# Optimization experiments

Hardware: AMD Instinct MI355X
Metric: run time of the kernel (lower is better)

Reference implementation:

```python
import jax, jax.numpy as jnp
import numpy as np
import math

HEADS = 16
HEAD_DIM = 64
MODEL_DIM = HEADS * HEAD_DIM
SEQ = 2048
BATCH = 2


def setup_inputs() -> dict:
    key = jax.random.key(0)
    ks = jax.random.split(key, 11)
    s = 0.02
    return {
        "query": jax.random.normal(ks[0], (SEQ, BATCH, MODEL_DIM), jnp.float32),
        "key": jax.random.normal(ks[1], (SEQ, BATCH, MODEL_DIM), jnp.float32),
        "value": jax.random.normal(ks[2], (SEQ, BATCH, MODEL_DIM), jnp.float32),
        "mask": jnp.ones((1, SEQ, 1), jnp.int32),
        "Wq": jax.random.normal(ks[3], (MODEL_DIM, MODEL_DIM), jnp.float32) * s,
        "bq": jax.random.normal(ks[4], (MODEL_DIM,), jnp.float32) * s,
        "Wk": jax.random.normal(ks[5], (MODEL_DIM, MODEL_DIM), jnp.float32) * s,
        "bk": jax.random.normal(ks[6], (MODEL_DIM,), jnp.float32) * s,
        "Wv": jax.random.normal(ks[7], (MODEL_DIM, MODEL_DIM), jnp.float32) * s,
        "bv": jax.random.normal(ks[8], (MODEL_DIM,), jnp.float32) * s,
        "Wo": jax.random.normal(ks[9], (MODEL_DIM, MODEL_DIM), jnp.float32) * s,
        "bo": jax.random.normal(ks[10], (MODEL_DIM,), jnp.float32) * s,
    }


def _proj(x, W, b):
    # torch nn.Linear: y = x @ W.T + b ; then view to [.., H, D]
    y = jnp.einsum("sbm,nm->sbn", x, W) + b
    return y.reshape(x.shape[0], x.shape[1], HEADS, HEAD_DIM)


def reference(query, key, value, mask, Wq, bq, Wk, bk, Wv, bv, Wo, bo):
    # NOTE: original module applies mask to `score` AFTER softmax has been
    # taken, and the masked score is discarded -> mask has no effect.
    del mask
    seq_len, batch_size, _ = query.shape
    scale = 1.0 / math.sqrt(HEAD_DIM)
    q = _proj(query, Wq, bq)   # [S,B,H,D]
    k = _proj(key, Wk, bk)
    v = _proj(value, Wv, bv)
    score = jnp.einsum("ibhd,jbhd->ijbh", q, k) * scale  # [S,S,B,H]
    attn = jax.nn.softmax(score, axis=1)  # softmax over key axis j
    # dropout: eval-mode identity (deterministic baseline)
    x = jnp.einsum("ijbh,jbhd->ibhd", attn, v)
    x = x.reshape(seq_len, batch_size, MODEL_DIM)
    return jnp.einsum("sbm,nm->sbn", x, Wo) + bo
```

## Files before the change

kernel.cpp:

```cpp
#include <hip/hip_runtime.h>

#define SEQ    2048
#define NBATCH 2
#define NHEAD  16
#define HD     64
#define MD     1024
#define TOK    (SEQ * NBATCH)
#define XN8    (TOK * MD / 8)
#define WN8    (MD * MD / 8)

typedef __attribute__((ext_vector_type(4)))  float f32x4;
typedef __attribute__((ext_vector_type(16))) float f32x16;
typedef __attribute__((ext_vector_type(8)))  short bf16x8;
typedef __attribute__((ext_vector_type(8)))  unsigned short u16x8;

__device__ __forceinline__ unsigned short f2bf(float f) {
  union { float f; unsigned int u; } x; x.f = f;
  unsigned int u = x.u + 0x7fffu + ((x.u >> 16) & 1u);
  return (unsigned short)(u >> 16);
}

__device__ __forceinline__ unsigned cvtpk(float lo, float hi) {
  unsigned r;
  asm("v_cvt_pk_bf16_f32 %0, %1, %2" : "=v"(r) : "v"(lo), "v"(hi));
  return r;
}
__device__ __forceinline__ void plswap(unsigned &a, unsigned &b) {
  asm volatile("v_permlane32_swap_b32 %0, %1" : "+v"(a), "+v"(b));
}

__device__ __forceinline__ void gload_lds16(const void* g, void* l) {
  typedef const __attribute__((address_space(1))) unsigned int* gp_t;
  typedef __attribute__((address_space(3))) unsigned int* lp_t;
  __builtin_amdgcn_global_load_lds((gp_t)g, (lp_t)l, 16, 0, 0);
}

__global__ __launch_bounds__(256) void cvt_all(
    const float* __restrict__ q, const float* __restrict__ k, const float* __restrict__ v,
    const float* __restrict__ wq, const float* __restrict__ wk,
    const float* __restrict__ wv, const float* __restrict__ wo,
    unsigned short* __restrict__ oq, unsigned short* __restrict__ ok,
    unsigned short* __restrict__ ov, unsigned short* __restrict__ owq,
    unsigned short* __restrict__ owk, unsigned short* __restrict__ owv,
    unsigned short* __restrict__ owo) {
  const int i = blockIdx.x * 256 + threadIdx.x;
  const float* src; unsigned short* dst; int r;
  if (i < 3 * XN8) {
    const int s = i >> 19; r = i & (XN8 - 1);
    src = s == 0 ? q : (s == 1 ? k : v);
    dst = s == 0 ? oq : (s == 1 ? ok : ov);
  } else {
    const int j = i - 3 * XN8; const int s = j >> 17; r = j & (WN8 - 1);
    src = s == 0 ? wq : (s == 1 ? wk : (s == 2 ? wv : wo));
    dst = s == 0 ? owq : (s == 1 ? owk : (s == 2 ? owv : owo));
  }
  const float4* p = (const float4*)src + (size_t)r * 2;
  float4 a = p[0];
  float4 b = p[1];
  u16x8 o;
  o[0] = f2bf(a.x); o[1] = f2bf(a.y); o[2] = f2bf(a.z); o[3] = f2bf(a.w);
  o[4] = f2bf(b.x); o[5] = f2bf(b.y); o[6] = f2bf(b.z); o[7] = f2bf(b.w);
  *((u16x8*)dst + r) = o;
}

__global__ __launch_bounds__(512) void gemm_qkv(
    const unsigned short* __restrict__ Xq, const unsigned short* __restrict__ Xk,
    const unsigned short* __restrict__ Xv, const unsigned short* __restrict__ Wq,
    const unsigned short* __restrict__ Wk, const unsigned short* __restrict__ Wv,
    const float* __restrict__ bq, const float* __restrict__ bk, const float* __restrict__ bv,
    unsigned short* __restrict__ Qo, unsigned short* __restrict__ Ko,
    unsigned short* __restrict__ Vo, float qscale) {
  __shared__ unsigned short sA[3][128 * 32];
  __shared__ unsigned short sB[3][128 * 32];
  const int tid  = threadIdx.x;
  const int lane = tid & 63;
  const int wave = tid >> 6;
  const int wm   = (wave >> 2) << 6;
  const int wn   = (wave & 3) << 5;
  const int l15  = lane & 15;
  const int g    = lane >> 4;
  const int z    = blockIdx.z;

  const unsigned short* A; const unsigned short* B; const float* bias;
  int bM, bN;
  if (z == 0)      { A = Xq; B = Wq; bias = bq; }
  else if (z == 1) { A = Xk; B = Wk; bias = bk; }
  else             { A = Wv; B = Xv; bias = bv; }
  if (z < 2) { bM = blockIdx.y << 7; bN = blockIdx.x << 7; }
  else       { bM = blockIdx.x << 7; bN = blockIdx.y << 7; }

  f32x4 acc[4][2];
#pragma unroll
  for (int a_ = 0; a_ < 4; ++a_)
#pragma unroll
    for (int b_ = 0; b_ < 2; ++b_)
      acc[a_][b_] = f32x4{0.f, 0.f, 0.f, 0.f};

  const int r = tid >> 2, cc = tid & 3;

  auto stage = [&](int c, int kt) {
    const int k0 = kt << 5;
    gload_lds16(A + (size_t)(bM + r) * MD + k0 + cc * 8, (char*)sA[c] + tid * 16);
    gload_lds16(B + (size_t)(bN + r) * MD + k0 + cc * 8, (char*)sB[c] + tid * 16);
  };

  const int nk = MD >> 5;
  stage(0, 0);
  stage(1, 1);
  asm volatile("s_waitcnt vmcnt(2)" ::: "memory");
  __builtin_amdgcn_s_barrier();

  int cur = 0;
  for (int kt = 0; kt < nk; ++kt) {
    if (kt + 2 < nk) stage(cur == 0 ? 2 : cur - 1, kt + 2);
    bf16x8 af[4], bfr[2];
#pragma unroll
    for (int f = 0; f < 4; ++f)
      af[f] = *(const bf16x8*)&sA[cur][(wm + f * 16 + l15) * 32 + g * 8];
#pragma unroll
    for (int f = 0; f < 2; ++f)
      bfr[f] = *(const bf16x8*)&sB[cur][(wn + f * 16 + l15) * 32 + g * 8];
#pragma unroll
    for (int mf = 0; mf < 4; ++mf)
#pragma unroll
      for (int nf = 0; nf < 2; ++nf)
        acc[mf][nf] = __builtin_amdgcn_mfma_f32_16x16x32_bf16(af[mf], bfr[nf], acc[mf][nf], 0, 0, 0);
    if (kt + 2 < nk)
      asm volatile("s_waitcnt vmcnt(2)" ::: "memory");
    else if (kt + 1 < nk)
      asm volatile("s_waitcnt vmcnt(0)" ::: "memory");
    if (kt + 1 < nk) __builtin_amdgcn_s_barrier();
    cur = (cur == 2) ? 0 : cur + 1;
  }

  if (z < 2) {
    unsigned short* O = (z == 0) ? Qo : Ko;
    const float scale = (z == 0) ? qscale : 1.0f;
#pragma unroll
    for (int nf = 0; nf < 2; ++nf) {
      const int cch = bN + wn + nf * 16 + l15;
      const float bb = bias[cch];
      const int h = cch >> 6, d = cch & 63;
#pragma unroll
      for (int mf = 0; mf < 4; ++mf)
#pragma unroll
        for (int i = 0; i < 4; ++i) {
          const int t = bM + wm + mf * 16 + (g << 2) + i;
          const int b = t & 1, s = t >> 1;
          O[((((b << 4) + h) * SEQ + s) << 6) + d] = f2bf((acc[mf][nf][i] + bb) * scale);
        }
    }
  } else {
#pragma unroll
    for (int mf = 0; mf < 4; ++mf)
#pragma unroll
      for (int i = 0; i < 4; ++i) {
        const int rch = bM + wm + mf * 16 + (g << 2) + i;
        const float bb = bias[rch];
        const int h = rch >> 6, d = rch & 63;
#pragma unroll
        for (int nf = 0; nf < 2; ++nf) {
          const int t = bN + wn + nf * 16 + l15;
          const int b = t & 1, s = t >> 1;
          Vo[((((b << 4) + h) << 6) + d) * SEQ + s] = f2bf(acc[mf][nf][i] + bb);
        }
      }
  }
}

__global__ __launch_bounds__(512) void gemm_oproj(const unsigned short* __restrict__ A,
                                                  const unsigned short* __restrict__ B,
                                                  const float* __restrict__ bias,
                                                  float* __restrict__ O) {
  __shared__ unsigned short sA[3][128 * 32];
  __shared__ unsigned short sB[3][128 * 32];
  const int tid  = threadIdx.x;
  const int lane = tid & 63;
  const int wave = tid >> 6;
  const int wm   = (wave >> 2) << 6;
  const int wn   = (wave & 3) << 5;
  const int l15  = lane & 15;
  const int g    = lane >> 4;
  const int bM   = blockIdx.y << 7;
  const int bN   = blockIdx.x << 7;

  f32x4 acc[4][2];
#pragma unroll
  for (int a_ = 0; a_ < 4; ++a_)
#pragma unroll
    for (int b_ = 0; b_ < 2; ++b_)
      acc[a_][b_] = f32x4{0.f, 0.f, 0.f, 0.f};

  const int r = tid >> 2, cc = tid & 3;
  auto stage = [&](int c, int kt) {
    const int k0 = kt << 5;
    gload_lds16(A + (size_t)(bM + r) * MD + k0 + cc * 8, (char*)sA[c] + tid * 16);
    gload_lds16(B + (size_t)(bN + r) * MD + k0 + cc * 8, (char*)sB[c] + tid * 16);
  };

  const int nk = MD >> 5;
  stage(0, 0);
  stage(1, 1);
  asm volatile("s_waitcnt vmcnt(2)" ::: "memory");
  __builtin_amdgcn_s_barrier();

  int cur = 0;
  for (int kt = 0; kt < nk; ++kt) {
    if (kt + 2 < nk) stage(cur == 0 ? 2 : cur - 1, kt + 2);
    bf16x8 af[4], bfr[2];
#pragma unroll
    for (int f = 0; f < 4; ++f)
      af[f] = *(const bf16x8*)&sA[cur][(wm + f * 16 + l15) * 32 + g * 8];
#pragma unroll
    for (int f = 0; f < 2; ++f)
      bfr[f] = *(const bf16x8*)&sB[cur][(wn + f * 16 + l15) * 32 + g * 8];
#pragma unroll
    for (int mf = 0; mf < 4; ++mf)
#pragma unroll
      for (int nf = 0; nf < 2; ++nf)
        acc[mf][nf] = __builtin_amdgcn_mfma_f32_16x16x32_bf16(af[mf], bfr[nf], acc[mf][nf], 0, 0, 0);
    if (kt + 2 < nk)
      asm volatile("s_waitcnt vmcnt(2)" ::: "memory");
    else if (kt + 1 < nk)
      asm volatile("s_waitcnt vmcnt(0)" ::: "memory");
    if (kt + 1 < nk) __builtin_amdgcn_s_barrier();
    cur = (cur == 2) ? 0 : cur + 1;
  }

#pragma unroll
  for (int nf = 0; nf < 2; ++nf) {
    const int cch = bN + wn + nf * 16 + l15;
    const float bb = bias[cch];
#pragma unroll
    for (int mf = 0; mf < 4; ++mf)
#pragma unroll
      for (int i = 0; i < 4; ++i) {
        const int t = bM + wm + mf * 16 + (g << 2) + i;
        O[(size_t)t * MD + cch] = acc[mf][nf][i] + bb;
      }
  }
}

__global__ __launch_bounds__(512) void attn_fwd(const unsigned short* __restrict__ Qg,
                                                const unsigned short* __restrict__ Kg,
                                                const unsigned short* __restrict__ Vg,
                                                unsigned short* __restrict__ Xout) {
  __shared__ unsigned short sK[2][2][64 * 64];
  __shared__ unsigned short sV[2][2][64 * 64];

  const int tid  = threadIdx.x;
  const int lane = tid & 63;
  const int wave = tid >> 6;
  const int ws   = wave & 3;
  const int grp  = wave >> 2;
  const int l31  = lane & 31;
  const int half = lane >> 5;
  const int bh   = blockIdx.y;
  const int q0w  = (blockIdx.x << 7) + (ws << 5);

  const unsigned short* Qb = Qg + (size_t)bh * (SEQ * HD);
  const char* Kb = (const char*)(Kg + (size_t)bh * (SEQ * HD));
  const char* Vb = (const char*)(Vg + (size_t)bh * (HD * SEQ));

  bf16x8 qf[4];
#pragma unroll
  for (int c = 0; c < 4; ++c)
    qf[c] = *(const bf16x8*)&Qb[(size_t)(q0w + l31) * HD + c * 16 + half * 8];

  f32x16 acc_o[2];
#pragma unroll
  for (int dt = 0; dt < 2; ++dt)
#pragma unroll
    for (int e = 0; e < 16; ++e) acc_o[dt][e] = 0.f;
  float lrow = 0.f;

  auto stage = [&](int c, int kt) {
#pragma unroll
    for (int h = 0; h < 2; ++h) {
      const int p = tid << 4;
      const int row = p >> 7;
      const int lcol = (p ^ ((row & 7) << 4)) & 127;
      const int kbase = (h << 10) + (kt << 6);
      gload_lds16(Kb + (size_t)(kbase + row) * (HD * 2) + lcol,
                  (char*)sK + ((h * 2 + c) << 13) + p);
      gload_lds16(Vb + (size_t)row * (SEQ * 2) + (kbase << 1) + lcol,
                  (char*)sV + ((h * 2 + c) << 13) + p);
    }
  };

  const char* myK = (char*)sK + (grp << 14);
  const char* myV = (char*)sV + (grp << 14);

  stage(0, 0);
  __syncthreads();
  int cur = 0;

  const int NT = SEQ / 2 / 64;
  for (int kt = 0; kt < NT; ++kt) {
    if (kt + 1 < NT) stage(cur ^ 1, kt + 1);

    f32x16 accs[2];
    __builtin_amdgcn_s_setprio(1);
#pragma unroll
    for (int ks = 0; ks < 2; ++ks) {
#pragma unroll
      for (int e = 0; e < 16; ++e) accs[ks][e] = 0.f;
      const int krow = ks * 32 + l31;
      const int swz  = (krow & 7) << 4;
#pragma unroll
      for (int c = 0; c < 4; ++c) {
        const int off = (krow << 7) + ((c * 32 + half * 16) ^ swz);
        bf16x8 kf = *(const bf16x8*)(myK + (cur << 13) + off);
        accs[ks] = __builtin_amdgcn_mfma_f32_32x32x16_bf16(kf, qf[c], accs[ks], 0, 0, 0);
      }
    }
    __builtin_amdgcn_s_setprio(0);

    float rsum = 0.f;
#pragma unroll
    for (int ks = 0; ks < 2; ++ks)
#pragma unroll
      for (int e = 0; e < 16; ++e) {
        const float pv = __builtin_amdgcn_exp2f(accs[ks][e]);
        accs[ks][e] = pv;
        rsum += pv;
      }
    lrow += rsum;

    bf16x8 pa[4];
#pragma unroll
    for (int ks = 0; ks < 2; ++ks)
#pragma unroll
      for (int hc = 0; hc < 2; ++hc) {
        const int b = hc * 8;
        unsigned X  = cvtpk(accs[ks][b + 0], accs[ks][b + 1]);
        unsigned X2 = cvtpk(accs[ks][b + 2], accs[ks][b + 3]);
        unsigned Y  = cvtpk(accs[ks][b + 4], accs[ks][b + 5]);
        unsigned Y2 = cvtpk(accs[ks][b + 6], accs[ks][b + 7]);
        plswap(X, Y);
        plswap(X2, Y2);
        union { unsigned u[4]; bf16x8 v; } w;
        w.u[0] = X; w.u[1] = X2; w.u[2] = Y; w.u[3] = Y2;
        pa[ks * 2 + hc] = w.v;
      }

    __builtin_amdgcn_s_setprio(1);
#pragma unroll
    for (int dt = 0; dt < 2; ++dt) {
      const int drow = dt * 32 + l31;
      const int swz  = (drow & 7) << 4;
#pragma unroll
      for (int kc = 0; kc < 4; ++kc) {
        const int off = (drow << 7) + ((kc * 32 + half * 16) ^ swz);
        bf16x8 vf = *(const bf16x8*)(myV + (cur << 13) + off);
        acc_o[dt] = __builtin_amdgcn_mfma_f32_32x32x16_bf16(vf, pa[kc], acc_o[dt], 0, 0, 0);
      }
    }
    __builtin_amdgcn_s_setprio(0);

    __syncthreads();
    cur ^= 1;
  }

  float lt = lrow + __shfl_xor(lrow, 32);
  float* dump  = (float*)sK;
  float* ldump = dump + 4 * 32 * 68;
  const int base = (ws * 32 + l31) * 68;

  if (grp == 1) {
#pragma unroll
    for (int dt = 0; dt < 2; ++dt)
#pragma unroll
      for (int r4 = 0; r4 < 4; ++r4) {
        const int d0 = dt * 32 + r4 * 8 + half * 4;
        const int e = r4 * 4;
        *(float2*)&dump[base + d0]     = float2{acc_o[dt][e + 0], acc_o[dt][e + 1]};
        *(float2*)&dump[base + d0 + 2] = float2{acc_o[dt][e + 2], acc_o[dt][e + 3]};
      }
    if (half == 0) ldump[ws * 32 + l31] = lt;
  }
  __syncthreads();
  if (grp == 0) {
    const float ltot = lt + ldump[ws * 32 + l31];
    const float inv = 1.f / ltot;
    const int b = bh >> 4, h = bh & 15;
    const int s = q0w + l31;
    const int t = s * NBATCH + b;
    unsigned short* Ot = Xout + (size_t)t * MD + (h << 6);
#pragma unroll
    for (int dt = 0; dt < 2; ++dt)
#pragma unroll
      for (int r4 = 0; r4 < 4; ++r4) {
        const int d0 = dt * 32 + r4 * 8 + half * 4;
        const int e = r4 * 4;
        float2 a0 = *(float2*)&dump[base + d0];
        float2 a1 = *(float2*)&dump[base + d0 + 2];
        uint2 w;
        w.x = cvtpk((acc_o[dt][e + 0] + a0.x) * inv, (acc_o[dt][e + 1] + a0.y) * inv);
        w.y = cvtpk((acc_o[dt][e + 2] + a1.x) * inv, (acc_o[dt][e + 3] + a1.y) * inv);
        *(uint2*)(Ot + d0) = w;
      }
  }
}

extern "C" void kernel_launch(void* const* d_in, const int* in_sizes, int n_in,
                              void* d_out, int out_size, void* d_ws, size_t ws_size,
                              hipStream_t stream) {
  const float* query = (const float*)d_in[0];
  const float* key   = (const float*)d_in[1];
  const float* value = (const float*)d_in[2];
  const float* Wq = (const float*)d_in[4];
  const float* bq = (const float*)d_in[5];
  const float* Wk = (const float*)d_in[6];
  const float* bk = (const float*)d_in[7];
  const float* Wv = (const float*)d_in[8];
  const float* bv = (const float*)d_in[9];
  const float* Wo = (const float*)d_in[10];
  const float* bo = (const float*)d_in[11];

  char* ws = (char*)d_ws;
  const size_t MB = 1024 * 1024;
  unsigned short* Xq  = (unsigned short*)(ws + 0 * MB);
  unsigned short* Xk  = (unsigned short*)(ws + 8 * MB);
  unsigned short* Xv  = (unsigned short*)(ws + 16 * MB);
  unsigned short* Wqb = (unsigned short*)(ws + 24 * MB);
  unsigned short* Wkb = (unsigned short*)(ws + 26 * MB);
  unsigned short* Wvb = (unsigned short*)(ws + 28 * MB);
  unsigned short* Wob = (unsigned short*)(ws + 30 * MB);
  unsigned short* Qb  = (unsigned short*)(ws + 32 * MB);
  unsigned short* Kb  = (unsigned short*)(ws + 40 * MB);
  unsigned short* Vb  = (unsigned short*)(ws + 48 * MB);
  unsigned short* Xa  = Xq;

  cvt_all<<<(3 * XN8 + 4 * WN8) / 256, 256, 0, stream>>>(
      query, key, value, Wq, Wk, Wv, Wo, Xq, Xk, Xv, Wqb, Wkb, Wvb, Wob);

  const float kQScale = 0.125f * 1.44269504088896340736f;
  dim3 gQKV(MD / 128, TOK / 128, 3);
  gemm_qkv<<<gQKV, 512, 0, stream>>>(Xq, Xk, Xv, Wqb, Wkb, Wvb,
                                     bq, bk, bv, Qb, Kb, Vb, kQScale);

  dim3 gA(SEQ / 128, NBATCH * NHEAD);
  attn_fwd<<<gA, 512, 0, stream>>>(Qb, Kb, Vb, Xa);

  dim3 gO(MD / 128, TOK / 128);
  gemm_oproj<<<gO, 512, 0, stream>>>(Xa, Wob, bo, (float*)d_out);
  (void)in_sizes; (void)n_in; (void)out_size; (void)ws_size;
}
```

Baseline: 121.7 us.

## Fuse fp32-to-bf16 activation conversion into QKV GEMM tile loading

The standalone conversion pass over the query, key and value activations is removed. The QKV GEMM now loads fp32 activation tiles into registers, packs them to bf16 with v_cvt_pk_bf16_f32, and writes them to LDS, while the weights still use direct global-to-LDS loads. This removes a full write and re-read of the bf16 activation copies. In exchange the GEMM reads twice the bytes per activation tile, passes them through VGPRs, and adds LDS-store waits to the pipeline, which could stall the K loop.

Result: slower. 134.9 us (+10.8%).

```diff
diff --git a/kernel.cpp b/kernel.cpp
--- a/kernel.cpp
+++ b/kernel.cpp
@@ -6,7 +6,6 @@
 #define HD     64
 #define MD     1024
 #define TOK    (SEQ * NBATCH)
-#define XN8    (TOK * MD / 8)
 #define WN8    (MD * MD / 8)
 
 typedef __attribute__((ext_vector_type(4)))  float f32x4;
@@ -35,25 +34,16 @@
   __builtin_amdgcn_global_load_lds((gp_t)g, (lp_t)l, 16, 0, 0);
 }
 
-__global__ __launch_bounds__(256) void cvt_all(
-    const float* __restrict__ q, const float* __restrict__ k, const float* __restrict__ v,
+__global__ __launch_bounds__(256) void cvt_w(
     const float* __restrict__ wq, const float* __restrict__ wk,
     const float* __restrict__ wv, const float* __restrict__ wo,
-    unsigned short* __restrict__ oq, unsigned short* __restrict__ ok,
-    unsigned short* __restrict__ ov, unsigned short* __restrict__ owq,
-    unsigned short* __restrict__ owk, unsigned short* __restrict__ owv,
-    unsigned short* __restrict__ owo) {
+    unsigned short* __restrict__ owq, unsigned short* __restrict__ owk,
+    unsigned short* __restrict__ owv, unsigned short* __restrict__ owo) {
   const int i = blockIdx.x * 256 + threadIdx.x;
-  const float* src; unsigned short* dst; int r;
-  if (i < 3 * XN8) {
-    const int s = i >> 19; r = i & (XN8 - 1);
-    src = s == 0 ? q : (s == 1 ? k : v);
-    dst = s == 0 ? oq : (s == 1 ? ok : ov);
-  } else {
-    const int j = i - 3 * XN8; const int s = j >> 17; r = j & (WN8 - 1);
-    src = s == 0 ? wq : (s == 1 ? wk : (s == 2 ? wv : wo));
-    dst = s == 0 ? owq : (s == 1 ? owk : (s == 2 ? owv : owo));
-  }
+  const int s = i >> 17;
+  const int r = i & (WN8 - 1);
+  const float* src = s == 0 ? wq : (s == 1 ? wk : (s == 2 ? wv : wo));
+  unsigned short* dst = s == 0 ? owq : (s == 1 ? owk : (s == 2 ? owv : owo));
   const float4* p = (const float4*)src + (size_t)r * 2;
   float4 a = p[0];
   float4 b = p[1];
@@ -64,8 +54,8 @@
 }
 
 __global__ __launch_bounds__(512) void gemm_qkv(
-    const unsigned short* __restrict__ Xq, const unsigned short* __restrict__ Xk,
-    const unsigned short* __restrict__ Xv, const unsigned short* __restrict__ Wq,
+    const float* __restrict__ Xq, const float* __restrict__ Xk,
+    const float* __restrict__ Xv, const unsigned short* __restrict__ Wq,
     const unsigned short* __restrict__ Wk, const unsigned short* __restrict__ Wv,
     const float* __restrict__ bq, const float* __restrict__ bk, const float* __restrict__ bv,
     unsigned short* __restrict__ Qo, unsigned short* __restrict__ Ko,
@@ -81,13 +71,17 @@
   const int g    = lane >> 4;
   const int z    = blockIdx.z;
 
-  const unsigned short* A; const unsigned short* B; const float* bias;
+  const float* Xf; const unsigned short* Wb; const float* bias;
+  if (z == 0)      { Xf = Xq; Wb = Wq; bias = bq; }
+  else if (z == 1) { Xf = Xk; Wb = Wk; bias = bk; }
+  else             { Xf = Xv; Wb = Wv; bias = bv; }
   int bM, bN;
-  if (z == 0)      { A = Xq; B = Wq; bias = bq; }
-  else if (z == 1) { A = Xk; B = Wk; bias = bk; }
-  else             { A = Wv; B = Xv; bias = bv; }
   if (z < 2) { bM = blockIdx.y << 7; bN = blockIdx.x << 7; }
   else       { bM = blockIdx.x << 7; bN = blockIdx.y << 7; }
+  const int bX = (z < 2) ? bM : bN;
+  const int bW = (z < 2) ? bN : bM;
+  unsigned short* sX3 = (z < 2) ? &sA[0][0] : &sB[0][0];
+  unsigned short* sW3 = (z < 2) ? &sB[0][0] : &sA[0][0];
 
   f32x4 acc[4][2];
 #pragma unroll
@@ -97,22 +91,44 @@
       acc[a_][b_] = f32x4{0.f, 0.f, 0.f, 0.f};
 
   const int r = tid >> 2, cc = tid & 3;
-
-  auto stage = [&](int c, int kt) {
-    const int k0 = kt << 5;
-    gload_lds16(A + (size_t)(bM + r) * MD + k0 + cc * 8, (char*)sA[c] + tid * 16);
-    gload_lds16(B + (size_t)(bN + r) * MD + k0 + cc * 8, (char*)sB[c] + tid * 16);
+  const float* xsrc = Xf + (size_t)(bX + r) * MD + cc * 8;
+  const unsigned short* wsrc = Wb + (size_t)(bW + r) * MD + cc * 8;
+
+  float4 ra, rb;
+  auto xissue = [&](int kt) {
+    ra = *(const float4*)(xsrc + (kt << 5));
+    rb = *(const float4*)(xsrc + (kt << 5) + 4);
   };
+  auto xwrite = [&](int c) {
+    union { unsigned u[4]; bf16x8 v; } w;
+    w.u[0] = cvtpk(ra.x, ra.y); w.u[1] = cvtpk(ra.z, ra.w);
+    w.u[2] = cvtpk(rb.x, rb.y); w.u[3] = cvtpk(rb.z, rb.w);
+    *(bf16x8*)(sX3 + c * 4096 + tid * 8) = w.v;
+  };
+  auto wissue = [&](int c, int kt) {
+    gload_lds16(wsrc + (kt << 5), (char*)(sW3 + c * 4096) + tid * 16);
+  };
 
   const int nk = MD >> 5;
-  stage(0, 0);
-  stage(1, 1);
-  asm volatile("s_waitcnt vmcnt(2)" ::: "memory");
+  xissue(0); wissue(0, 0);
+  asm volatile("s_waitcnt vmcnt(1)" ::: "memory");
+  xwrite(0);
+  xissue(1); wissue(1, 1);
+  asm volatile("s_waitcnt vmcnt(3)" ::: "memory");
+  asm volatile("s_waitcnt lgkmcnt(0)" ::: "memory");
   __builtin_amdgcn_s_barrier();
 
   int cur = 0;
   for (int kt = 0; kt < nk; ++kt) {
-    if (kt + 2 < nk) stage(cur == 0 ? 2 : cur - 1, kt + 2);
+    const int nxt = (cur == 2) ? 0 : cur + 1;
+    if (kt + 1 < nk) {
+      asm volatile("s_waitcnt vmcnt(1)" ::: "memory");
+      xwrite(nxt);
+    }
+    if (kt + 2 < nk) {
+      const int nn = (nxt == 2) ? 0 : nxt + 1;
+      xissue(kt + 2); wissue(nn, kt + 2);
+    }
     bf16x8 af[4], bfr[2];
 #pragma unroll
     for (int f = 0; f < 4; ++f)
@@ -125,12 +141,15 @@
 #pragma unroll
       for (int nf = 0; nf < 2; ++nf)
         acc[mf][nf] = __builtin_amdgcn_mfma_f32_16x16x32_bf16(af[mf], bfr[nf], acc[mf][nf], 0, 0, 0);
-    if (kt + 2 < nk)
-      asm volatile("s_waitcnt vmcnt(2)" ::: "memory");
-    else if (kt + 1 < nk)
-      asm volatile("s_waitcnt vmcnt(0)" ::: "memory");
-    if (kt + 1 < nk) __builtin_amdgcn_s_barrier();
-    cur = (cur == 2) ? 0 : cur + 1;
+    if (kt + 1 < nk) {
+      if (kt + 2 < nk)
+        asm volatile("s_waitcnt vmcnt(3)" ::: "memory");
+      else
+        asm volatile("s_waitcnt vmcnt(0)" ::: "memory");
+      asm volatile("s_waitcnt lgkmcnt(0)" ::: "memory");
+      __builtin_amdgcn_s_barrier();
+    }
+    cur = nxt;
   }
 
   if (z < 2) {
@@ -420,9 +439,7 @@
 
   char* ws = (char*)d_ws;
   const size_t MB = 1024 * 1024;
-  unsigned short* Xq  = (unsigned short*)(ws + 0 * MB);
-  unsigned short* Xk  = (unsigned short*)(ws + 8 * MB);
-  unsigned short* Xv  = (unsigned short*)(ws + 16 * MB);
+  unsigned short* Xa  = (unsigned short*)(ws + 0 * MB);
   unsigned short* Wqb = (unsigned short*)(ws + 24 * MB);
   unsigned short* Wkb = (unsigned short*)(ws + 26 * MB);
   unsigned short* Wvb = (unsigned short*)(ws + 28 * MB);
@@ -430,14 +447,12 @@
   unsigned short* Qb  = (unsigned short*)(ws + 32 * MB);
   unsigned short* Kb  = (unsigned short*)(ws + 40 * MB);
   unsigned short* Vb  = (unsigned short*)(ws + 48 * MB);
-  unsigned short* Xa  = Xq;
-
-  cvt_all<<<(3 * XN8 + 4 * WN8) / 256, 256, 0, stream>>>(
-      query, key, value, Wq, Wk, Wv, Wo, Xq, Xk, Xv, Wqb, Wkb, Wvb, Wob);
+
+  cvt_w<<<4 * WN8 / 256, 256, 0, stream>>>(Wq, Wk, Wv, Wo, Wqb, Wkb, Wvb, Wob);
 
   const float kQScale = 0.125f * 1.44269504088896340736f;
   dim3 gQKV(MD / 128, TOK / 128, 3);
-  gemm_qkv<<<gQKV, 512, 0, stream>>>(Xq, Xk, Xv, Wqb, Wkb, Wvb,
+  gemm_qkv<<<gQKV, 512, 0, stream>>>(query, key, value, Wqb, Wkb, Wvb,
                                      bq, bk, bv, Qb, Kb, Vb, kQScale);
 
   dim3 gA(SEQ / 128, NBATCH * NHEAD);
```
